# Kernel tuning notes

Hardware: AMD Instinct MI355X
Metric: run time of the kernel (lower is better)

Reference implementation:

```python
import jax, jax.numpy as jnp
import numpy as np

H = 100      # hidden size
L = 4096     # sequence length


def setup_inputs() -> dict:
    key = jax.random.key(0)
    ks = jax.random.split(key, 11)
    s = 1.0 / np.sqrt(H)
    u = lambda k, sh: jax.random.uniform(k, sh, jnp.float32, -s, s)
    return {
        "input_seq": jax.random.normal(ks[0], (L,), jnp.float32),
        "W_ih_l0": u(ks[1], (4 * H, 1)),
        "W_hh_l0": u(ks[2], (4 * H, H)),
        "b_ih_l0": u(ks[3], (4 * H,)),
        "b_hh_l0": u(ks[4], (4 * H,)),
        "W_ih_l1": u(ks[5], (4 * H, H)),
        "W_hh_l1": u(ks[6], (4 * H, H)),
        "b_ih_l1": u(ks[7], (4 * H,)),
        "b_hh_l1": u(ks[8], (4 * H,)),
        "W_lin": u(ks[9], (1, H)),
        "b_lin": u(ks[10], (1,)),
    }


def _lstm_layer(x, Wih, Whh, bih, bhh):
    # x: [L, B, in] -> hs: [L, B, H]. PyTorch gate order: i, f, g, o.
    h_dim = Wih.shape[0] // 4
    b = bih + bhh

    def step(carry, xt):
        h, c = carry
        gates = xt @ Wih.T + h @ Whh.T + b          # [B, 4H]
        i, f, g, o = jnp.split(gates, 4, axis=-1)
        c = jax.nn.sigmoid(f) * c + jax.nn.sigmoid(i) * jnp.tanh(g)
        h = jax.nn.sigmoid(o) * jnp.tanh(c)
        return (h, c), h

    B = x.shape[1]
    h0 = jnp.zeros((B, h_dim), x.dtype)
    c0 = jnp.zeros((B, h_dim), x.dtype)
    _, hs = jax.lax.scan(step, (h0, c0), x)
    return hs


def reference(input_seq, W_ih_l0, W_hh_l0, b_ih_l0, b_hh_l0,
              W_ih_l1, W_hh_l1, b_ih_l1, b_hh_l1, W_lin, b_lin):
    x = input_seq.reshape(-1, 1, 1)                 # [L, B=1, 1]
    h1 = _lstm_layer(x, W_ih_l0, W_hh_l0, b_ih_l0, b_hh_l0)   # [L,1,H]
    h2 = _lstm_layer(h1, W_ih_l1, W_hh_l1, b_ih_l1, b_hh_l1)  # [L,1,H]
    preds = h2.reshape(h2.shape[0], -1) @ W_lin.T + b_lin      # [L,1]
    return preds[-1]                                 # [1]
```

## Files before the change

kernel.cpp:

```cpp
#include <hip/hip_runtime.h>

#define HH 100
#define LL 4096
#define NT 512

#define WS_H1_FLOATS (LL*128)
#define WS_NEEDED ((size_t)WS_H1_FLOATS*4 + (size_t)LL*4)

typedef float v2f __attribute__((ext_vector_type(2)));
__device__ __forceinline__ v2f fma2(v2f a, v2f b, v2f c) { return __builtin_elementwise_fma(a, b, c); }
__device__ __forceinline__ v2f v2c(float2 f) { v2f r; r.x = f.x; r.y = f.y; return r; }

__device__ __forceinline__ float sigmoidf_(float x) { return 1.0f / (1.0f + __expf(-x)); }
__device__ __forceinline__ float tanhf_(float x)    { return 1.0f - 2.0f / (__expf(2.0f * x) + 1.0f); }

#define DECLROW(n) v2f n##_0,n##_1,n##_2,n##_3,n##_4,n##_5,n##_6,n##_7,n##_8,n##_9,n##_10,n##_11, \
                       n##_12,n##_13,n##_14,n##_15,n##_16,n##_17,n##_18,n##_19,n##_20,n##_21,n##_22,n##_23,n##_24;
#define LOADROW(n, P) { const float2* q2_ = reinterpret_cast<const float2*>(P); \
  n##_0=v2c(q2_[0]);   n##_1=v2c(q2_[1]);   n##_2=v2c(q2_[2]);   n##_3=v2c(q2_[3]);   n##_4=v2c(q2_[4]); \
  n##_5=v2c(q2_[5]);   n##_6=v2c(q2_[6]);   n##_7=v2c(q2_[7]);   n##_8=v2c(q2_[8]);   n##_9=v2c(q2_[9]); \
  n##_10=v2c(q2_[10]); n##_11=v2c(q2_[11]); n##_12=v2c(q2_[12]); n##_13=v2c(q2_[13]); n##_14=v2c(q2_[14]); \
  n##_15=v2c(q2_[15]); n##_16=v2c(q2_[16]); n##_17=v2c(q2_[17]); n##_18=v2c(q2_[18]); n##_19=v2c(q2_[19]); \
  n##_20=v2c(q2_[20]); n##_21=v2c(q2_[21]); n##_22=v2c(q2_[22]); n##_23=v2c(q2_[23]); n##_24=v2c(q2_[24]); }

#define STEP2(j,p,q) { float4 hv = hb4[j]; v2f hl, hh; hl.x=hv.x; hl.y=hv.y; hh.x=hv.z; hh.y=hv.w; \
  a0=fma2(wa_##p,hl,a0); a0=fma2(wa_##q,hh,a0); \
  a1=fma2(wb_##p,hl,a1); a1=fma2(wb_##q,hh,a1); }

#define STEP4(j,p,q) { float4 hv = hb4[j]; v2f hl, hh; hl.x=hv.x; hl.y=hv.y; hh.x=hv.z; hh.y=hv.w; \
  a0=fma2(wa_##p,hl,a0); a0=fma2(wa_##q,hh,a0); \
  a1=fma2(wb_##p,hl,a1); a1=fma2(wb_##q,hh,a1); \
  a2=fma2(wc_##p,hl,a2); a2=fma2(wc_##q,hh,a2); \
  a3=fma2(wd_##p,hl,a3); a3=fma2(wd_##q,hh,a3); }

#define P_LDS_FLOATS 5120

__global__ __attribute__((amdgpu_flat_work_group_size(NT, NT)))
           __attribute__((amdgpu_waves_per_eu(2, 2)))
void lstm_pipe2(const float* __restrict__ x_seq,  const float* __restrict__ Wih0,
                const float* __restrict__ Whh0,   const float* __restrict__ bih0,
                const float* __restrict__ bhh0,   const float* __restrict__ Wih1,
                const float* __restrict__ Whh1,   const float* __restrict__ bih1,
                const float* __restrict__ bhh1,   const float* __restrict__ Wlin,
                const float* __restrict__ blin,   float* __restrict__ ws_h1,
                int* __restrict__ ws_flag,        float* __restrict__ out)
{
    extern __shared__ float lds[];
    const int tid = threadIdx.x;

    if (blockIdx.x == 0) {
        float* x_s   = lds;
        float* h1_s  = lds + 4096;
        float* part0 = lds + 4200;

        const int half = tid & 1;
        const int q    = tid >> 1;
        const bool act = (q < 200);
        const int r0   = act ? 2*q : 0;

        {   const float4* src = reinterpret_cast<const float4*>(x_seq);
            float4* dst = reinterpret_cast<float4*>(x_s);
            for (int i = tid; i < LL/4; i += NT) dst[i] = src[i]; }
        if (tid < 104) h1_s[tid] = 0.0f;

        DECLROW(wa) DECLROW(wb)
        LOADROW(wa, Whh0 + (r0+0)*HH + half*50)
        LOADROW(wb, Whh0 + (r0+1)*HH + half*50)
        float bw0 = 0.f, bw1 = 0.f;
        if (act) {
            if (half == 0) { bw0 = bih0[r0] + bhh0[r0]; bw1 = bih0[r0+1] + bhh0[r0+1]; }
            else           { bw0 = Wih0[r0];            bw1 = Wih0[r0+1]; }
        }
        const float4* hb4 = reinterpret_cast<const float4*>(h1_s + half*52);
        float c0 = 0.0f;
        __syncthreads();

        for (int t = 0; t < LL; ++t) {
            const float xt  = x_s[t];
            const float xvs = half ? xt : 1.0f;
            if (act) {
                v2f a0 = {0.f,0.f}, a1 = {0.f,0.f};
                STEP2(0,0,1)   STEP2(1,2,3)   STEP2(2,4,5)   STEP2(3,6,7)
                STEP2(4,8,9)   STEP2(5,10,11) STEP2(6,12,13) STEP2(7,14,15)
                STEP2(8,16,17) STEP2(9,18,19) STEP2(10,20,21) STEP2(11,22,23)
                { float4 hv = hb4[12]; v2f hl; hl.x = hv.x; hl.y = hv.y;
                  a0 = fma2(wa_24, hl, a0); a1 = fma2(wb_24, hl, a1); }
                float* pw = part0 + half*400 + r0;
                pw[0] = fmaf(bw0, xvs, a0.x + a0.y);
                pw[1] = fmaf(bw1, xvs, a1.x + a1.y);
            }
            __syncthreads();
            if (tid < 100) {
                const int j = tid;
                float G0 = part0[j]       + part0[400 + j];
                float G1 = part0[j + 100] + part0[500 + j];
                float G2 = part0[j + 200] + part0[600 + j];
                float G3 = part0[j + 300] + part0[700 + j];
                c0 = sigmoidf_(G1)*c0 + sigmoidf_(G0)*tanhf_(G2);
                float h = sigmoidf_(G3)*tanhf_(c0);
                h1_s[j + 2*(j >= 50)] = h;
                __hip_atomic_store(&ws_h1[t*128 + j], h, __ATOMIC_RELAXED, __HIP_MEMORY_SCOPE_AGENT);
            }
            __syncthreads();
            if (tid == 0)
                __hip_atomic_store(&ws_flag[t], 1, __ATOMIC_RELEASE, __HIP_MEMORY_SCOPE_AGENT);
        }
    } else {
        float* h1c   = lds;
        float* h2_s  = lds + 104;
        float* part1 = lds + 208;
        float* red   = lds + 1808;

        const bool dotter = (tid < 400);
        const int  c    = dotter ? (tid / 200) : 0;
        const int  rem  = dotter ? (tid % 200) : 0;
        const int  half = rem / 100;
        const int  b    = rem % 100;
        const int  rb   = 4*b;
        const float* mat = c ? Whh1 : Wih1;

        DECLROW(wa) DECLROW(wb) DECLROW(wc) DECLROW(wd)
        LOADROW(wa, mat + (rb+0)*HH + half*50)
        LOADROW(wb, mat + (rb+1)*HH + half*50)
        LOADROW(wc, mat + (rb+2)*HH + half*50)
        LOADROW(wd, mat + (rb+3)*HH + half*50)
        float bw0=0.f, bw1=0.f, bw2=0.f, bw3=0.f;
        if (dotter && c == 0 && half == 0) {
            bw0 = bih1[rb]   + bhh1[rb];
            bw1 = bih1[rb+1] + bhh1[rb+1];
            bw2 = bih1[rb+2] + bhh1[rb+2];
            bw3 = bih1[rb+3] + bhh1[rb+3];
        }
        const float4* hb4 = reinterpret_cast<const float4*>((c ? h2_s : h1c) + half*52);
        const int pbase = half*800 + c*400 + rb;

        const bool gl = (tid >= 400) && (tid < 500);
        const int  j  = tid - 400;
        const float wl = gl ? Wlin[j] : 0.0f;
        float c1 = 0.0f;

        if (tid < 104) { h1c[tid] = 0.0f; h2_s[tid] = 0.0f; }
        __syncthreads();
        if (gl) {
            while (__hip_atomic_load(&ws_flag[0], __ATOMIC_ACQUIRE, __HIP_MEMORY_SCOPE_AGENT) == 0) {}
            float h0 = __hip_atomic_load(&ws_h1[j], __ATOMIC_RELAXED, __HIP_MEMORY_SCOPE_AGENT);
            h1c[j + 2*(j >= 50)] = h0;
            while (__hip_atomic_load(&ws_flag[1], __ATOMIC_ACQUIRE, __HIP_MEMORY_SCOPE_AGENT) == 0) {}
        }
        __syncthreads();

        for (int t = 0; t < LL; ++t) {
            float hnf = 0.0f; int f2v = 1;
            if (gl) {
                const int tp1 = (t+1 < LL) ? t+1 : LL-1;
                const int tp2 = (t+2 < LL) ? t+2 : LL-1;
                hnf = __hip_atomic_load(&ws_h1[tp1*128 + j], __ATOMIC_RELAXED, __HIP_MEMORY_SCOPE_AGENT);
                f2v = __hip_atomic_load(&ws_flag[tp2], __ATOMIC_ACQUIRE, __HIP_MEMORY_SCOPE_AGENT);
            }
            if (dotter) {
                v2f a0 = {0.f,0.f}, a1 = {0.f,0.f}, a2 = {0.f,0.f}, a3 = {0.f,0.f};
                STEP4(0,0,1)   STEP4(1,2,3)   STEP4(2,4,5)   STEP4(3,6,7)
                STEP4(4,8,9)   STEP4(5,10,11) STEP4(6,12,13) STEP4(7,14,15)
                STEP4(8,16,17) STEP4(9,18,19) STEP4(10,20,21) STEP4(11,22,23)
                { float4 hv = hb4[12]; v2f hl; hl.x = hv.x; hl.y = hv.y;
                  a0 = fma2(wa_24, hl, a0); a1 = fma2(wb_24, hl, a1);
                  a2 = fma2(wc_24, hl, a2); a3 = fma2(wd_24, hl, a3); }
                reinterpret_cast<float4*>(part1 + pbase)[0] =
                    make_float4(a0.x + a0.y + bw0, a1.x + a1.y + bw1,
                                a2.x + a2.y + bw2, a3.x + a3.y + bw3);
            }
            __syncthreads();
            if (gl) {
                float G0 = (part1[j]       + part1[800+j])       + (part1[400+j]       + part1[1200+j]);
                float G1 = (part1[j+100]   + part1[900+j])       + (part1[500+j]       + part1[1300+j]);
                float G2 = (part1[j+200]   + part1[1000+j])      + (part1[600+j]       + part1[1400+j]);
                float G3 = (part1[j+300]   + part1[1100+j])      + (part1[700+j]       + part1[1500+j]);
                c1 = sigmoidf_(G1)*c1 + sigmoidf_(G0)*tanhf_(G2);
                h2_s[j + 2*(j >= 50)] = sigmoidf_(G3)*tanhf_(c1);
                h1c[j + 2*(j >= 50)] = hnf;
                while (f2v == 0) {
                    const int tp2 = (t+2 < LL) ? t+2 : LL-1;
                    f2v = __hip_atomic_load(&ws_flag[tp2], __ATOMIC_ACQUIRE, __HIP_MEMORY_SCOPE_AGENT);
                }
            }
            __syncthreads();
        }
        if (gl) red[j] = wl * h2_s[j + 2*(j >= 50)];
        __syncthreads();
        if (tid == 0) {
            float s = blin[0];
            for (int k = 0; k < HH; ++k) s += red[k];
            out[0] = s;
        }
    }
}

#define NLDSROW 176
#define RB0  176
#define WQ_OFF   4096
#define H1_OFF   (WQ_OFF + 2*NLDSROW*52)
#define H2_OFF   (H1_OFF + 104)
#define PART_OFF (H2_OFF + 104)
#define Q_OFF    (PART_OFF + 2048)
#define LDS_FLOATS (Q_OFF + 352)

#define TSK(j) { float4 wv = tp4[j]; float4 hv = hb4t[j]; v2f wl_,wh_,hl_,hh_; \
  wl_.x=wv.x; wl_.y=wv.y; wh_.x=wv.z; wh_.y=wv.w; hl_.x=hv.x; hl_.y=hv.y; hh_.x=hv.z; hh_.y=hv.w; \
  tq=fma2(wl_,hl_,tq); tq=fma2(wh_,hh_,tq); }

__global__ __attribute__((amdgpu_flat_work_group_size(NT, NT)))
           __attribute__((amdgpu_waves_per_eu(2, 2)))
void lstm_v256_kernel(const float* __restrict__ x_seq, const float* __restrict__ Wih0,
                      const float* __restrict__ Whh0,  const float* __restrict__ bih0,
                      const float* __restrict__ bhh0,  const float* __restrict__ Wih1,
                      const float* __restrict__ Whh1,  const float* __restrict__ bih1,
                      const float* __restrict__ bhh1,  const float* __restrict__ Wlin,
                      const float* __restrict__ blin,  float* __restrict__ out)
{
    extern __shared__ float lds[];
    float* x_s    = lds;
    float* wq     = lds + WQ_OFF;
    float* h1_s   = lds + H1_OFF;
    float* h2_s   = lds + H2_OFF;
    float* part_s = lds + PART_OFF;
    float* q_s    = lds + Q_OFF;

    const int tid  = threadIdx.x;
    const int half = tid & 1;
    const int qid  = tid >> 1;
    const int rowbase = RB0 + 4*qid;

    {   const float4* src = reinterpret_cast<const float4*>(x_seq);
        float4* dst = reinterpret_cast<float4*>(x_s);
        for (int i = tid; i < LL/4; i += NT) dst[i] = src[i]; }
    for (int idx = tid; idx < 2*NLDSROW*50; idx += NT) {
        int hf  = idx / (NLDSROW*50);
        int rem = idx - hf*(NLDSROW*50);
        int row = rem / 50;
        int cc  = rem - row*50;
        wq[(hf*NLDSROW + row)*52 + cc] = Whh0[row*HH + hf*50 + cc];
    }
    if (tid < 104) { h1_s[tid] = 0.0f; h2_s[tid] = 0.0f; }

    const float* M; int r0;
    if (rowbase < 400)      { M = Whh0; r0 = rowbase; }
    else if (rowbase < 800) { M = Wih1; r0 = rowbase - 400; }
    else                    { M = Whh1; r0 = rowbase - 800; }

    DECLROW(wa) DECLROW(wb) DECLROW(wc) DECLROW(wd)
    LOADROW(wa, M + (r0+0)*HH + half*50)
    LOADROW(wb, M + (r0+1)*HH + half*50)
    LOADROW(wc, M + (r0+2)*HH + half*50)
    LOADROW(wd, M + (r0+3)*HH + half*50)

    float bw0, bw1, bw2, bw3;
    {
        const int ra = rowbase, rb = rowbase+1, rc = rowbase+2, rd = rowbase+3;
        if (half == 0) {
            bw0 = (ra < 400) ? (bih0[ra] + bhh0[ra]) : (ra < 800) ? (bih1[ra-400] + bhh1[ra-400]) : 0.0f;
            bw1 = (rb < 400) ? (bih0[rb] + bhh0[rb]) : (rb < 800) ? (bih1[rb-400] + bhh1[rb-400]) : 0.0f;
            bw2 = (rc < 400) ? (bih0[rc] + bhh0[rc]) : (rc < 800) ? (bih1[rc-400] + bhh1[rc-400]) : 0.0f;
            bw3 = (rd < 400) ? (bih0[rd] + bhh0[rd]) : (rd < 800) ? (bih1[rd-400] + bhh1[rd-400]) : 0.0f;
        } else {
            bw0 = (ra < 400) ? Wih0[ra] : 0.0f;
            bw1 = (rb < 400) ? Wih0[rb] : 0.0f;
            bw2 = (rc < 400) ? Wih0[rc] : 0.0f;
            bw3 = (rd < 400) ? Wih0[rd] : 0.0f;
        }
    }

    float lb = 0.0f;
    if (tid < 2*NLDSROW) lb = half ? Wih0[qid] : (bih0[qid] + bhh0[qid]);
    const float4* tp4  = reinterpret_cast<const float4*>(wq + (half*NLDSROW + qid)*52);
    const float4* hb4t = reinterpret_cast<const float4*>(h1_s + half*52);
    const float4* hb4  = reinterpret_cast<const float4*>(((rowbase < 800) ? h1_s : h2_s) + half*52);

    const float wl = (tid < HH) ? Wlin[tid] : 0.0f;
    const int slotbase = qid + half*1024;
    float c0 = 0.0f, c1 = 0.0f;
    __syncthreads();

    for (int t = 0; t <= LL; ++t) {
        const float xt  = x_s[(t < LL) ? t : (LL-1)];
        const float xvs = half ? xt : 1.0f;
        {
            v2f a0 = {0.f,0.f}, a1 = {0.f,0.f}, a2 = {0.f,0.f}, a3 = {0.f,0.f};
            STEP4(0,0,1)   STEP4(1,2,3)   STEP4(2,4,5)   STEP4(3,6,7)
            STEP4(4,8,9)   STEP4(5,10,11) STEP4(6,12,13) STEP4(7,14,15)
            STEP4(8,16,17) STEP4(9,18,19) STEP4(10,20,21) STEP4(11,22,23)
            { float4 hv = hb4[12]; v2f hl; hl.x = hv.x; hl.y = hv.y;
              a0 = fma2(wa_24, hl, a0); a1 = fma2(wb_24, hl, a1);
              a2 = fma2(wc_24, hl, a2); a3 = fma2(wd_24, hl, a3); }
            part_s[slotbase + 0*256] = fmaf(bw0, xvs, a0.x + a0.y);
            part_s[slotbase + 1*256] = fmaf(bw1, xvs, a1.x + a1.y);
            part_s[slotbase + 2*256] = fmaf(bw2, xvs, a2.x + a2.y);
            part_s[slotbase + 3*256] = fmaf(bw3, xvs, a3.x + a3.y);
        }
        if (tid < 2*NLDSROW) {
            v2f tq = {0.f,0.f};
            TSK(0) TSK(1) TSK(2) TSK(3) TSK(4) TSK(5)
            TSK(6) TSK(7) TSK(8) TSK(9) TSK(10) TSK(11)
            { float4 wv = tp4[12]; float4 hv = hb4t[12];
              v2f wl_, hl_; wl_.x = wv.x; wl_.y = wv.y; hl_.x = hv.x; hl_.y = hv.y;
              tq = fma2(wl_, hl_, tq); }
            q_s[qid + half*NLDSROW] = fmaf(lb, xvs, tq.x + tq.y);
        }
        __syncthreads();
        if (tid < HH) {
            const int jj = tid;
            float g[4];
            #pragma unroll
            for (int k = 0; k < 4; ++k) {
                int r = jj + k*100;
                if (r < NLDSROW) g[k] = q_s[r] + q_s[r + NLDSROW];
                else { int rr = r - RB0; int bb = (rr >> 2) + ((rr & 3) << 8);
                       g[k] = part_s[bb] + part_s[bb + 1024]; }
            }
            if (t < LL) {
                c0 = sigmoidf_(g[1])*c0 + sigmoidf_(g[0])*tanhf_(g[2]);
                h1_s[jj + 2*(jj >= 50)] = sigmoidf_(g[3])*tanhf_(c0);
            }
        } else if (tid >= 128 && tid < 128 + HH) {
            if (t >= 1) {
                const int jj = tid - 128;
                float v[4];
                #pragma unroll
                for (int k = 0; k < 4; ++k) {
                    int g1i = jj + k*100;
                    int rr1 = (400 + g1i) - RB0; int b1i = (rr1 >> 2) + ((rr1 & 3) << 8);
                    int rr2 = (800 + g1i) - RB0; int b2i = (rr2 >> 2) + ((rr2 & 3) << 8);
                    v[k] = (part_s[b1i] + part_s[b1i + 1024]) + (part_s[b2i] + part_s[b2i + 1024]);
                }
                c1 = sigmoidf_(v[1])*c1 + sigmoidf_(v[0])*tanhf_(v[2]);
                h2_s[jj + 2*(jj >= 50)] = sigmoidf_(v[3])*tanhf_(c1);
            }
        }
        __syncthreads();
    }
    if (tid < HH) part_s[tid] = wl * h2_s[tid + 2*(tid >= 50)];
    __syncthreads();
    if (tid == 0) {
        float s = 0.0f;
        for (int k = 0; k < HH; ++k) s += part_s[k];
        out[0] = s + blin[0];
    }
}

extern "C" void kernel_launch(void* const* d_in, const int* in_sizes, int n_in,
                              void* d_out, int out_size, void* d_ws, size_t ws_size,
                              hipStream_t stream) {
    (void)in_sizes; (void)n_in; (void)out_size;

    const float* x_seq = (const float*)d_in[0];
    const float* Wih0  = (const float*)d_in[1];
    const float* Whh0  = (const float*)d_in[2];
    const float* bih0  = (const float*)d_in[3];
    const float* bhh0  = (const float*)d_in[4];
    const float* Wih1  = (const float*)d_in[5];
    const float* Whh1  = (const float*)d_in[6];
    const float* bih1  = (const float*)d_in[7];
    const float* bhh1  = (const float*)d_in[8];
    const float* Wlin  = (const float*)d_in[9];
    const float* blin  = (const float*)d_in[10];
    float* out = (float*)d_out;

    if (d_ws != nullptr && ws_size >= WS_NEEDED) {
        float* ws_h1  = (float*)d_ws;
        int*   ws_flg = (int*)((char*)d_ws + (size_t)WS_H1_FLOATS*4);
        hipMemsetAsync(ws_flg, 0, LL*sizeof(int), stream);
        hipLaunchKernelGGL(lstm_pipe2, dim3(2), dim3(NT),
                           P_LDS_FLOATS*sizeof(float), stream,
                           x_seq, Wih0, Whh0, bih0, bhh0,
                           Wih1, Whh1, bih1, bhh1, Wlin, blin,
                           ws_h1, ws_flg, out);
    } else {
        static bool attr_set = false;
        if (!attr_set) {
            hipFuncSetAttribute((const void*)lstm_v256_kernel,
                                hipFuncAttributeMaxDynamicSharedMemorySize,
                                LDS_FLOATS * (int)sizeof(float));
            attr_set = true;
        }
        hipLaunchKernelGGL(lstm_v256_kernel, dim3(1), dim3(NT),
                           LDS_FLOATS * sizeof(float), stream,
                           x_seq, Wih0, Whh0, bih0, bhh0,
                           Wih1, Whh1, bih1, bhh1, Wlin, blin, out);
    }
}
```

Measured before the change: 4.281 ms.

## Use LDS-only barriers and deferred flag publish with deeper consumer prefetch

Replaces __syncthreads in both pipeline stages with a custom barrier that waits only on LDS counters, so outstanding global stores no longer stall every step. The producer publishes the flag for step t-1 one iteration later, after an explicit vmcnt wait on the storing threads, in place of a release store right after a second barrier. The consumer prefetches layer-1 hidden states three steps ahead with a two-deep register queue and uses relaxed flag loads. This risks memory-ordering subtleties, since the release semantics now rest on manual waitcnt instead of atomic ordering.

```diff
diff --git a/kernel.cpp b/kernel.cpp
--- a/kernel.cpp
+++ b/kernel.cpp
@@ -13,6 +13,13 @@
 
 __device__ __forceinline__ float sigmoidf_(float x) { return 1.0f / (1.0f + __expf(-x)); }
 __device__ __forceinline__ float tanhf_(float x)    { return 1.0f - 2.0f / (__expf(2.0f * x) + 1.0f); }
+
+__device__ __forceinline__ void wg_barrier_lds() {
+    __builtin_amdgcn_sched_barrier(0);
+    asm volatile("s_waitcnt lgkmcnt(0)" ::: "memory");
+    __builtin_amdgcn_s_barrier();
+    __builtin_amdgcn_sched_barrier(0);
+}
 
 #define DECLROW(n) v2f n##_0,n##_1,n##_2,n##_3,n##_4,n##_5,n##_6,n##_7,n##_8,n##_9,n##_10,n##_11, \
                        n##_12,n##_13,n##_14,n##_15,n##_16,n##_17,n##_18,n##_19,n##_20,n##_21,n##_22,n##_23,n##_24;
@@ -23,27 +30,40 @@
   n##_15=v2c(q2_[15]); n##_16=v2c(q2_[16]); n##_17=v2c(q2_[17]); n##_18=v2c(q2_[18]); n##_19=v2c(q2_[19]); \
   n##_20=v2c(q2_[20]); n##_21=v2c(q2_[21]); n##_22=v2c(q2_[22]); n##_23=v2c(q2_[23]); n##_24=v2c(q2_[24]); }
 
-#define STEP2(j,p,q) { float4 hv = hb4[j]; v2f hl, hh; hl.x=hv.x; hl.y=hv.y; hh.x=hv.z; hh.y=hv.w; \
-  a0=fma2(wa_##p,hl,a0); a0=fma2(wa_##q,hh,a0); \
-  a1=fma2(wb_##p,hl,a1); a1=fma2(wb_##q,hh,a1); }
-
-#define STEP4(j,p,q) { float4 hv = hb4[j]; v2f hl, hh; hl.x=hv.x; hl.y=hv.y; hh.x=hv.z; hh.y=hv.w; \
-  a0=fma2(wa_##p,hl,a0); a0=fma2(wa_##q,hh,a0); \
-  a1=fma2(wb_##p,hl,a1); a1=fma2(wb_##q,hh,a1); \
-  a2=fma2(wc_##p,hl,a2); a2=fma2(wc_##q,hh,a2); \
-  a3=fma2(wd_##p,hl,a3); a3=fma2(wd_##q,hh,a3); }
+#define STEP2(j,p,q) { float4 hv = hb4[j]; v2f hlo, hhi; hlo.x=hv.x; hlo.y=hv.y; hhi.x=hv.z; hhi.y=hv.w; \
+  a0=fma2(wa_##p,hlo,a0); a0=fma2(wa_##q,hhi,a0); \
+  a1=fma2(wb_##p,hlo,a1); a1=fma2(wb_##q,hhi,a1); }
+#define DOT2ALL  STEP2(0,0,1) STEP2(1,2,3) STEP2(2,4,5) STEP2(3,6,7) STEP2(4,8,9) STEP2(5,10,11) \
+                 STEP2(6,12,13) STEP2(7,14,15) STEP2(8,16,17) STEP2(9,18,19) STEP2(10,20,21) STEP2(11,22,23) \
+                 { float4 hv = hb4[12]; v2f hlo; hlo.x=hv.x; hlo.y=hv.y; \
+                   a0=fma2(wa_24,hlo,a0); a1=fma2(wb_24,hlo,a1); }
+
+#define STEP4(j,p,q) { float4 hv = hb4[j]; v2f hlo, hhi; hlo.x=hv.x; hlo.y=hv.y; hhi.x=hv.z; hhi.y=hv.w; \
+  a0=fma2(wa_##p,hlo,a0); a0=fma2(wa_##q,hhi,a0); \
+  a1=fma2(wb_##p,hlo,a1); a1=fma2(wb_##q,hhi,a1); \
+  a2=fma2(wc_##p,hlo,a2); a2=fma2(wc_##q,hhi,a2); \
+  a3=fma2(wd_##p,hlo,a3); a3=fma2(wd_##q,hhi,a3); }
+#define DOT4ALL  STEP4(0,0,1) STEP4(1,2,3) STEP4(2,4,5) STEP4(3,6,7) STEP4(4,8,9) STEP4(5,10,11) \
+                 STEP4(6,12,13) STEP4(7,14,15) STEP4(8,16,17) STEP4(9,18,19) STEP4(10,20,21) STEP4(11,22,23) \
+                 { float4 hv = hb4[12]; v2f hlo; hlo.x=hv.x; hlo.y=hv.y; \
+                   a0=fma2(wa_24,hlo,a0); a1=fma2(wb_24,hlo,a1); \
+                   a2=fma2(wc_24,hlo,a2); a3=fma2(wd_24,hlo,a3); }
+
+#define AST(p,v)   __hip_atomic_store((p), (v), __ATOMIC_RELAXED, __HIP_MEMORY_SCOPE_AGENT)
+#define ALD(p)     __hip_atomic_load((p), __ATOMIC_RELAXED, __HIP_MEMORY_SCOPE_AGENT)
+#define AFLAGLD(p) __hip_atomic_load((p), __ATOMIC_ACQUIRE, __HIP_MEMORY_SCOPE_AGENT)
 
 #define P_LDS_FLOATS 5120
 
 __global__ __attribute__((amdgpu_flat_work_group_size(NT, NT)))
            __attribute__((amdgpu_waves_per_eu(2, 2)))
-void lstm_pipe2(const float* __restrict__ x_seq,  const float* __restrict__ Wih0,
-                const float* __restrict__ Whh0,   const float* __restrict__ bih0,
-                const float* __restrict__ bhh0,   const float* __restrict__ Wih1,
-                const float* __restrict__ Whh1,   const float* __restrict__ bih1,
-                const float* __restrict__ bhh1,   const float* __restrict__ Wlin,
-                const float* __restrict__ blin,   float* __restrict__ ws_h1,
-                int* __restrict__ ws_flag,        float* __restrict__ out)
+void lstm_pipe2c(const float* __restrict__ x_seq,  const float* __restrict__ Wih0,
+                 const float* __restrict__ Whh0,   const float* __restrict__ bih0,
+                 const float* __restrict__ bhh0,   const float* __restrict__ Wih1,
+                 const float* __restrict__ Whh1,   const float* __restrict__ bih1,
+                 const float* __restrict__ bhh1,   const float* __restrict__ Wlin,
+                 const float* __restrict__ blin,   float* __restrict__ ws_h1,
+                 int* __restrict__ ws_flag,        float* __restrict__ out)
 {
     extern __shared__ float lds[];
     const int tid = threadIdx.x;
@@ -80,16 +100,14 @@
             const float xvs = half ? xt : 1.0f;
             if (act) {
                 v2f a0 = {0.f,0.f}, a1 = {0.f,0.f};
-                STEP2(0,0,1)   STEP2(1,2,3)   STEP2(2,4,5)   STEP2(3,6,7)
-                STEP2(4,8,9)   STEP2(5,10,11) STEP2(6,12,13) STEP2(7,14,15)
-                STEP2(8,16,17) STEP2(9,18,19) STEP2(10,20,21) STEP2(11,22,23)
-                { float4 hv = hb4[12]; v2f hl; hl.x = hv.x; hl.y = hv.y;
-                  a0 = fma2(wa_24, hl, a0); a1 = fma2(wb_24, hl, a1); }
+                DOT2ALL
                 float* pw = part0 + half*400 + r0;
                 pw[0] = fmaf(bw0, xvs, a0.x + a0.y);
                 pw[1] = fmaf(bw1, xvs, a1.x + a1.y);
             }
-            __syncthreads();
+            if (tid < 100 && t > 0) asm volatile("s_waitcnt vmcnt(0)" ::: "memory");
+            wg_barrier_lds();
+            if (tid == 0 && t > 0) AST(&ws_flag[t-1], 1);
             if (tid < 100) {
                 const int j = tid;
                 float G0 = part0[j]       + part0[400 + j];
@@ -99,12 +117,13 @@
                 c0 = sigmoidf_(G1)*c0 + sigmoidf_(G0)*tanhf_(G2);
                 float h = sigmoidf_(G3)*tanhf_(c0);
                 h1_s[j + 2*(j >= 50)] = h;
-                __hip_atomic_store(&ws_h1[t*128 + j], h, __ATOMIC_RELAXED, __HIP_MEMORY_SCOPE_AGENT);
-            }
-            __syncthreads();
-            if (tid == 0)
-                __hip_atomic_store(&ws_flag[t], 1, __ATOMIC_RELEASE, __HIP_MEMORY_SCOPE_AGENT);
-        }
+                AST(&ws_h1[t*128 + j], h);
+            }
+            wg_barrier_lds();
+        }
+        if (tid < 100) asm volatile("s_waitcnt vmcnt(0)" ::: "memory");
+        __syncthreads();
+        if (tid == 0) AST(&ws_flag[LL-1], 1);
     } else {
         float* h1c   = lds;
         float* h2_s  = lds + 104;
@@ -138,52 +157,45 @@
         const int  j  = tid - 400;
         const float wl = gl ? Wlin[j] : 0.0f;
         float c1 = 0.0f;
+        float hn1 = 0.0f, hn2 = 0.0f;
 
         if (tid < 104) { h1c[tid] = 0.0f; h2_s[tid] = 0.0f; }
         __syncthreads();
         if (gl) {
-            while (__hip_atomic_load(&ws_flag[0], __ATOMIC_ACQUIRE, __HIP_MEMORY_SCOPE_AGENT) == 0) {}
-            float h0 = __hip_atomic_load(&ws_h1[j], __ATOMIC_RELAXED, __HIP_MEMORY_SCOPE_AGENT);
-            h1c[j + 2*(j >= 50)] = h0;
-            while (__hip_atomic_load(&ws_flag[1], __ATOMIC_ACQUIRE, __HIP_MEMORY_SCOPE_AGENT) == 0) {}
+            while (AFLAGLD(&ws_flag[0]) == 0) {}
+            h1c[j + 2*(j >= 50)] = ALD(&ws_h1[j]);
+            while (AFLAGLD(&ws_flag[1]) == 0) {}
+            hn1 = ALD(&ws_h1[128 + j]);
+            while (AFLAGLD(&ws_flag[2]) == 0) {}
+            hn2 = ALD(&ws_h1[256 + j]);
         }
         __syncthreads();
 
         for (int t = 0; t < LL; ++t) {
-            float hnf = 0.0f; int f2v = 1;
-            if (gl) {
-                const int tp1 = (t+1 < LL) ? t+1 : LL-1;
-                const int tp2 = (t+2 < LL) ? t+2 : LL-1;
-                hnf = __hip_atomic_load(&ws_h1[tp1*128 + j], __ATOMIC_RELAXED, __HIP_MEMORY_SCOPE_AGENT);
-                f2v = __hip_atomic_load(&ws_flag[tp2], __ATOMIC_ACQUIRE, __HIP_MEMORY_SCOPE_AGENT);
-            }
+            const int tp3 = (t+3 < LL) ? t+3 : LL-1;
+            int f3 = 1;
+            if (gl) f3 = ALD(&ws_flag[tp3]);
             if (dotter) {
                 v2f a0 = {0.f,0.f}, a1 = {0.f,0.f}, a2 = {0.f,0.f}, a3 = {0.f,0.f};
-                STEP4(0,0,1)   STEP4(1,2,3)   STEP4(2,4,5)   STEP4(3,6,7)
-                STEP4(4,8,9)   STEP4(5,10,11) STEP4(6,12,13) STEP4(7,14,15)
-                STEP4(8,16,17) STEP4(9,18,19) STEP4(10,20,21) STEP4(11,22,23)
-                { float4 hv = hb4[12]; v2f hl; hl.x = hv.x; hl.y = hv.y;
-                  a0 = fma2(wa_24, hl, a0); a1 = fma2(wb_24, hl, a1);
-                  a2 = fma2(wc_24, hl, a2); a3 = fma2(wd_24, hl, a3); }
+                DOT4ALL
                 reinterpret_cast<float4*>(part1 + pbase)[0] =
                     make_float4(a0.x + a0.y + bw0, a1.x + a1.y + bw1,
                                 a2.x + a2.y + bw2, a3.x + a3.y + bw3);
             }
-            __syncthreads();
+            wg_barrier_lds();
             if (gl) {
-                float G0 = (part1[j]       + part1[800+j])       + (part1[400+j]       + part1[1200+j]);
-                float G1 = (part1[j+100]   + part1[900+j])       + (part1[500+j]       + part1[1300+j]);
-                float G2 = (part1[j+200]   + part1[1000+j])      + (part1[600+j]       + part1[1400+j]);
-                float G3 = (part1[j+300]   + part1[1100+j])      + (part1[700+j]       + part1[1500+j]);
+                float G0 = (part1[j]       + part1[800+j])  + (part1[400+j]  + part1[1200+j]);
+                float G1 = (part1[j+100]   + part1[900+j])  + (part1[500+j]  + part1[1300+j]);
+                float G2 = (part1[j+200]   + part1[1000+j]) + (part1[600+j]  + part1[1400+j]);
+                float G3 = (part1[j+300]   + part1[1100+j]) + (part1[700+j]  + part1[1500+j]);
                 c1 = sigmoidf_(G1)*c1 + sigmoidf_(G0)*tanhf_(G2);
                 h2_s[j + 2*(j >= 50)] = sigmoidf_(G3)*tanhf_(c1);
-                h1c[j + 2*(j >= 50)] = hnf;
-                while (f2v == 0) {
-                    const int tp2 = (t+2 < LL) ? t+2 : LL-1;
-                    f2v = __hip_atomic_load(&ws_flag[tp2], __ATOMIC_ACQUIRE, __HIP_MEMORY_SCOPE_AGENT);
-                }
-            }
-            __syncthreads();
+                h1c[j + 2*(j >= 50)] = hn1;
+                hn1 = hn2;
+                while (f3 == 0) f3 = ALD(&ws_flag[tp3]);
+                hn2 = ALD(&ws_h1[tp3*128 + j]);
+            }
+            wg_barrier_lds();
         }
         if (gl) red[j] = wl * h2_s[j + 2*(j >= 50)];
         __syncthreads();
@@ -234,11 +246,11 @@
         float4* dst = reinterpret_cast<float4*>(x_s);
         for (int i = tid; i < LL/4; i += NT) dst[i] = src[i]; }
     for (int idx = tid; idx < 2*NLDSROW*50; idx += NT) {
-        int hf  = idx / (NLDSROW*50);
-        int rem = idx - hf*(NLDSROW*50);
+        int hfx = idx / (NLDSROW*50);
+        int rem = idx - hfx*(NLDSROW*50);
         int row = rem / 50;
         int cc  = rem - row*50;
-        wq[(hf*NLDSROW + row)*52 + cc] = Whh0[row*HH + hf*50 + cc];
+        wq[(hfx*NLDSROW + row)*52 + cc] = Whh0[row*HH + hfx*50 + cc];
     }
     if (tid < 104) { h1_s[tid] = 0.0f; h2_s[tid] = 0.0f; }
 
@@ -285,12 +297,7 @@
         const float xvs = half ? xt : 1.0f;
         {
             v2f a0 = {0.f,0.f}, a1 = {0.f,0.f}, a2 = {0.f,0.f}, a3 = {0.f,0.f};
-            STEP4(0,0,1)   STEP4(1,2,3)   STEP4(2,4,5)   STEP4(3,6,7)
-            STEP4(4,8,9)   STEP4(5,10,11) STEP4(6,12,13) STEP4(7,14,15)
-            STEP4(8,16,17) STEP4(9,18,19) STEP4(10,20,21) STEP4(11,22,23)
-            { float4 hv = hb4[12]; v2f hl; hl.x = hv.x; hl.y = hv.y;
-              a0 = fma2(wa_24, hl, a0); a1 = fma2(wb_24, hl, a1);
-              a2 = fma2(wc_24, hl, a2); a3 = fma2(wd_24, hl, a3); }
+            DOT4ALL
             part_s[slotbase + 0*256] = fmaf(bw0, xvs, a0.x + a0.y);
             part_s[slotbase + 1*256] = fmaf(bw1, xvs, a1.x + a1.y);
             part_s[slotbase + 2*256] = fmaf(bw2, xvs, a2.x + a2.y);
@@ -368,7 +375,7 @@
         float* ws_h1  = (float*)d_ws;
         int*   ws_flg = (int*)((char*)d_ws + (size_t)WS_H1_FLOATS*4);
         hipMemsetAsync(ws_flg, 0, LL*sizeof(int), stream);
-        hipLaunchKernelGGL(lstm_pipe2, dim3(2), dim3(NT),
+        hipLaunchKernelGGL(lstm_pipe2c, dim3(2), dim3(NT),
                            P_LDS_FLOATS*sizeof(float), stream,
                            x_seq, Wih0, Whh0, bih0, bhh0,
                            Wih1, Whh1, bih1, bhh1, Wlin, blin,
```

New measurement: 4.378 ms. 1.02x slower.
